# Optimization experiments

Hardware: AMD Instinct MI355X
Metric: run time of the kernel (lower is better)

## Reference

```python
import jax, jax.numpy as jnp
import numpy as np

V = 1024      # visible_size (channel_size)
H = 2048      # hidden_size
F = V + H     # full_size
T = 64        # timesteps
REC = 0.8     # params['lambda']


def setup_inputs() -> dict:
    key = jax.random.key(0)
    k1, k2, k3 = jax.random.split(key, 3)
    X = jax.random.normal(k1, (T, V), jnp.float32)
    # scale W so tanh does not fully saturate (fan-in scaling, like default init)
    W = jax.random.normal(k2, (F, F), jnp.float32) / np.float32(np.sqrt(F))
    b = jax.random.normal(k3, (F,), jnp.float32) * 0.01
    # Lambda: visible block = REC, hidden block = 1, diagonal of visible block = 1
    lam = jnp.concatenate(
        [jnp.full((V, V), REC, jnp.float32), jnp.ones((V, H), jnp.float32)], axis=1
    )
    lam = lam.at[jnp.arange(V), jnp.arange(V)].set(1.0)
    return {"X": X, "W": W, "b": b, "lam": lam}


def reference(X, W, b, lam):
    v = lam.shape[0]           # visible size
    one_minus_lam_vis = 1.0 - lam[:, :v]  # zero outside visible block anyway

    def step(carry, x_t):
        R, _ = carry
        WR = R @ W.T + b                      # [V, F] Linear applied row-wise
        U = lam * WR                          # gated recurrent part
        # I has x_t broadcast across rows in the visible block, zeros elsewhere
        U = U.at[:, :v].add(one_minus_lam_vis * x_t[None, :])
        R_next = jnp.tanh(U)                  # phi = torch.tanh
        return (R_next, U), None

    R0 = jnp.zeros((v, W.shape[0]), X.dtype)
    (_, U_last), _ = jax.lax.scan(step, (R0, R0), X)
    # torch.diag(U[:, :visible]) -> diagonal entries, shape [V]
    idx = jnp.arange(v)
    return U_last[idx, idx]
```

## Files before the change

kernel.cpp:

```cpp
#include <hip/hip_runtime.h>
#include <math.h>

#define V 1024
#define H 2048
#define F 3072
#define T 64
#define REC 0.8f

#define BM 128
#define BN 128
#define KT16 (F / 16)
#define NSS  (KT16 / 4)

typedef _Float16 half8 __attribute__((ext_vector_type(8)));
typedef float floatx16 __attribute__((ext_vector_type(16)));

__device__ __forceinline__ void gld16(const void* g, void* l) {
    __builtin_amdgcn_global_load_lds(
        (const __attribute__((address_space(1))) void*)g,
        (__attribute__((address_space(3))) void*)l, 16, 0, 0);
}

__device__ __forceinline__ float fast_tanh(float u) {
    float e = __expf(2.f * u);
    return 1.f - 2.f * __builtin_amdgcn_rcpf(e + 1.f);
}


__global__ __launch_bounds__(256)
void conv_w_fm(const float* __restrict__ W, _Float16* __restrict__ Wfm) {
    const int ct = blockIdx.y;
    const int ix = blockIdx.x * 256 + threadIdx.x;
    const int kt = ix >> 8;
    const int q  = ix & 255;
    const int n  = ct * 128 + ((q >> 6) & 3) * 32 + (q & 31);
    const int k0 = kt * 16 + ((q >> 5) & 1) * 8;
    const float* src = W + (size_t)n * F + k0;
    float4 v0 = *(const float4*)src;
    float4 v1 = *(const float4*)(src + 4);
    half8 o = { (_Float16)v0.x, (_Float16)v0.y, (_Float16)v0.z, (_Float16)v0.w,
                (_Float16)v1.x, (_Float16)v1.y, (_Float16)v1.z, (_Float16)v1.w };
    *(half8*)(Wfm + ((size_t)(ct * KT16 + kt) * 2048 + q * 8)) = o;
}

__global__ __launch_bounds__(256)
void init_step0(const float* __restrict__ b, const float* __restrict__ x0,
                _Float16* __restrict__ Rfm) {
    const int rt = blockIdx.y;
    const int ix = blockIdx.x * 256 + threadIdx.x;
    const int kt = ix >> 8;
    const int q  = ix & 255;
    const int gi = rt * 128 + ((q >> 6) & 3) * 32 + (q & 31);
    const int k0 = kt * 16 + ((q >> 5) & 1) * 8;
    half8 o;
    #pragma unroll
    for (int e = 0; e < 8; ++e) {
        int gj = k0 + e;
        float wr = b[gj];
        float u = (gj >= V || gi == gj) ? wr : (REC * wr + (1.f - REC) * x0[gj]);
        o[e] = (_Float16)fast_tanh(u);
    }
    *(half8*)(Rfm + ((size_t)(rt * KT16 + kt) * 2048 + q * 8)) = o;
}

__global__ __launch_bounds__(512, 2)
void frnn_step(const _Float16* __restrict__ Rin, const _Float16* __restrict__ Wfm,
               const float* __restrict__ b, const float* __restrict__ xt,
               _Float16* __restrict__ Rout, float* __restrict__ out, int is_last)
{
    __shared__ _Float16 A0[8192], B0[8192];
    __shared__ _Float16 A1[8192], B1[8192];
    __shared__ _Float16 A2[8192], B2[8192];

    const int tid  = threadIdx.x;
    const int lane = tid & 63;
    const int wid  = tid >> 6;
    const int sp   = wid & 1;
    const int kg   = wid >> 1;
    const int row0 = blockIdx.y * BM;
    const int col0 = blockIdx.x * BN;
    const int lane8 = lane * 8;

    const int sq  = tid & 255;
    const int sq8 = sq * 8;
    const _Float16* sgbase = (tid < 256)
        ? Rin + ((size_t)blockIdx.y * KT16 * 2048 + sq8)
        : Wfm + ((size_t)blockIdx.x * KT16 * 2048 + sq8);

    floatx16 acc[2][4];
    #pragma unroll
    for (int i = 0; i < 2; ++i)
        #pragma unroll
        for (int j = 0; j < 4; ++j)
            #pragma unroll
            for (int r = 0; r < 16; ++r) acc[i][j][r] = 0.f;

    {
        _Float16* d0 = (tid < 256) ? &A0[sq8] : &B0[sq8];
        _Float16* d1 = (tid < 256) ? &A1[sq8] : &B1[sq8];
        #pragma unroll
        for (int g = 0; g < 4; ++g)
            gld16(sgbase + (size_t)g * 2048, d0 + g * 2048);
        asm volatile("" ::: "memory");
        #pragma unroll
        for (int g = 0; g < 4; ++g)
            gld16(sgbase + (size_t)(4 + g) * 2048, d1 + g * 2048);
    }

#define BODY(M, CA, CB, NA, NB)                                                 \
  {                                                                             \
    asm volatile("s_waitcnt vmcnt(4) lgkmcnt(0)\n\ts_barrier" ::: "memory");    \
    const _Float16* sA = &CA[kg * 2048];                                        \
    const _Float16* sB = &CB[kg * 2048];                                        \
    half8 a0 = *(const half8*)(sA + sp * 1024 + lane8);                         \
    half8 a1 = *(const half8*)(sA + sp * 1024 + 512 + lane8);                   \
    half8 b0 = *(const half8*)(sB + lane8);                                     \
    half8 b1 = *(const half8*)(sB + 512 + lane8);                               \
    half8 b2 = *(const half8*)(sB + 1024 + lane8);                              \
    half8 b3 = *(const half8*)(sB + 1536 + lane8);                              \
    asm volatile("" ::: "memory");           \
    int nxt = (M) + 2; if (nxt >= NSS) nxt -= NSS;     \
    _Float16* dst = (tid < 256) ? &NA[sq8] : &NB[sq8];                          \
    _Pragma("unroll")                                                           \
    for (int g = 0; g < 4; ++g)                                                 \
        gld16(sgbase + (size_t)(nxt * 4 + g) * 2048, dst + g * 2048);           \
    acc[0][0] = __builtin_amdgcn_mfma_f32_32x32x16_f16(a0, b0, acc[0][0],0,0,0);\
    acc[0][1] = __builtin_amdgcn_mfma_f32_32x32x16_f16(a0, b1, acc[0][1],0,0,0);\
    acc[0][2] = __builtin_amdgcn_mfma_f32_32x32x16_f16(a0, b2, acc[0][2],0,0,0);\
    acc[0][3] = __builtin_amdgcn_mfma_f32_32x32x16_f16(a0, b3, acc[0][3],0,0,0);\
    acc[1][0] = __builtin_amdgcn_mfma_f32_32x32x16_f16(a1, b0, acc[1][0],0,0,0);\
    acc[1][1] = __builtin_amdgcn_mfma_f32_32x32x16_f16(a1, b1, acc[1][1],0,0,0);\
    acc[1][2] = __builtin_amdgcn_mfma_f32_32x32x16_f16(a1, b2, acc[1][2],0,0,0);\
    acc[1][3] = __builtin_amdgcn_mfma_f32_32x32x16_f16(a1, b3, acc[1][3],0,0,0);\
  }

    #pragma unroll 1
    for (int m3 = 0; m3 < NSS / 3; ++m3) {
        const int M = m3 * 3;
        BODY(M,     A0, B0, A2, B2)
        BODY(M + 1, A1, B1, A0, B0)
        BODY(M + 2, A2, B2, A1, B1)
    }
#undef BODY

    asm volatile("s_waitcnt vmcnt(0) lgkmcnt(0)\n\ts_barrier" ::: "memory");

    const int m32 = lane & 31, hh = lane >> 5;
    float b_r[4], x_r[4];
    if (kg == 0) {
        #pragma unroll
        for (int j = 0; j < 4; ++j) {
            int gj = col0 + j * 32 + m32;
            b_r[j] = b[gj];
            x_r[j] = (gj < V) ? xt[gj] : 0.f;
        }
    }

    float* red0 = (float*)(sp ? A1 : A0);
    float* red1 = (float*)(sp ? B1 : B0);
    #pragma unroll 1
    for (int w = 1; w < 4; ++w) {
        if (kg == w) {
            #pragma unroll
            for (int j = 0; j < 4; ++j)
                #pragma unroll
                for (int q4 = 0; q4 < 4; ++q4) {
                    float4 v0 = { acc[0][j][4*q4],   acc[0][j][4*q4+1],
                                  acc[0][j][4*q4+2], acc[0][j][4*q4+3] };
                    float4 v1 = { acc[1][j][4*q4],   acc[1][j][4*q4+1],
                                  acc[1][j][4*q4+2], acc[1][j][4*q4+3] };
                    *(float4*)(red0 + (j*4 + q4) * 256 + lane * 4) = v0;
                    *(float4*)(red1 + (j*4 + q4) * 256 + lane * 4) = v1;
                }
        }
        __syncthreads();
        if (kg == 0) {
            #pragma unroll
            for (int j = 0; j < 4; ++j)
                #pragma unroll
                for (int q4 = 0; q4 < 4; ++q4) {
                    float4 v0 = *(const float4*)(red0 + (j*4 + q4) * 256 + lane * 4);
                    float4 v1 = *(const float4*)(red1 + (j*4 + q4) * 256 + lane * 4);
                    acc[0][j][4*q4]   += v0.x; acc[0][j][4*q4+1] += v0.y;
                    acc[0][j][4*q4+2] += v0.z; acc[0][j][4*q4+3] += v0.w;
                    acc[1][j][4*q4]   += v1.x; acc[1][j][4*q4+1] += v1.y;
                    acc[1][j][4*q4+2] += v1.z; acc[1][j][4*q4+3] += v1.w;
                }
        }
        __syncthreads();
    }

    if (kg == 0) {
        #pragma unroll
        for (int i = 0; i < 2; ++i) {
            const int mb = sp * 2 + i;
            #pragma unroll
            for (int j = 0; j < 4; ++j) {
                const int gj = col0 + j * 32 + m32;
                const int kt = gj >> 4;
                const int h2 = (gj >> 3) & 1;
                const int e  = gj & 7;
                _Float16* tb = Rout + ((size_t)(blockIdx.y * KT16 + kt) * 2048
                                       + (mb * 2 + h2) * 256 + e);
                const float bj = b_r[j];
                const float xj = x_r[j];
                const bool vis = (gj < V);
                #pragma unroll
                for (int r = 0; r < 16; ++r) {
                    const int mrow = 4 * hh + (r & 3) + 8 * (r >> 2);
                    const int gi = row0 + mb * 32 + mrow;
                    float wr = acc[i][j][r] + bj;
                    float u = (!vis || gi == gj) ? wr : (REC * wr + (1.f - REC) * xj);
                    tb[mrow * 8] = (_Float16)fast_tanh(u);
                    if (is_last && gi == gj) out[gi] = u;
                }
            }
        }
    }
}

extern "C" void kernel_launch(void* const* d_in, const int* in_sizes, int n_in,
                              void* d_out, int out_size, void* d_ws, size_t ws_size,
                              hipStream_t stream) {
    const float* X = (const float*)d_in[0];
    const float* W = (const float*)d_in[1];
    const float* b = (const float*)d_in[2];
    float* out = (float*)d_out;

    _Float16* Wfm = (_Float16*)d_ws;
    _Float16* Ra  = Wfm + (size_t)F * F;
    _Float16* Rb  = Ra + (size_t)V * F;

    conv_w_fm<<<dim3(192, 24), 256, 0, stream>>>(W, Wfm);
    init_step0<<<dim3(192, 8), 256, 0, stream>>>(b, X, Ra);

    for (int t = 1; t < T; ++t) {
        _Float16* Rin  = (t & 1) ? Ra : Rb;
        _Float16* Rout = (t & 1) ? Rb : Ra;
        frnn_step<<<dim3(24, 8), 512, 0, stream>>>(Rin, Wfm, b, X + (size_t)t * V,
                                                   Rout, out, t == T - 1);
    }
}
```

Before: 2.082 ms.

## Double-buffer LDS fragments in registers and deepen global prefetch to three stages

Adds a register-level double buffer: each iteration loads the next stage's A/B fragments from LDS while issuing MFMAs on fragments loaded in the previous iteration. The global-to-LDS prefetch distance grows from two to three stages, the main loop is unrolled by six to rotate both buffers, and MFMA issue is wrapped in s_setprio and a sched_barrier. The aim is to hide LDS read latency behind the matrix cores, at the cost of more VGPRs and possible occupancy loss. With three LDS buffers and a prefetch distance of three, the buffer being refilled may still be read by lagging waves, since the barrier only covers the previous stage.

```diff
diff --git a/kernel.cpp b/kernel.cpp
--- a/kernel.cpp
+++ b/kernel.cpp
@@ -95,6 +95,8 @@
             #pragma unroll
             for (int r = 0; r < 16; ++r) acc[i][j][r] = 0.f;
 
+    half8 fa0[2], fa1[2], fb0[2], fb1[2], fb2[2], fb3[2];
+
     {
         _Float16* d0 = (tid < 256) ? &A0[sq8] : &B0[sq8];
         _Float16* d1 = (tid < 256) ? &A1[sq8] : &B1[sq8];
@@ -105,41 +107,65 @@
         #pragma unroll
         for (int g = 0; g < 4; ++g)
             gld16(sgbase + (size_t)(4 + g) * 2048, d1 + g * 2048);
-    }
-
-#define BODY(M, CA, CB, NA, NB)                                                 \
+        asm volatile("" ::: "memory");
+    }
+    {
+        asm volatile("s_waitcnt vmcnt(4) lgkmcnt(0)\n\ts_barrier" ::: "memory");
+        const _Float16* sA = &A0[kg * 2048];
+        const _Float16* sB = &B0[kg * 2048];
+        fa0[0] = *(const half8*)(sA + sp * 1024 + lane8);
+        fa1[0] = *(const half8*)(sA + sp * 1024 + 512 + lane8);
+        fb0[0] = *(const half8*)(sB + lane8);
+        fb1[0] = *(const half8*)(sB + 512 + lane8);
+        fb2[0] = *(const half8*)(sB + 1024 + lane8);
+        fb3[0] = *(const half8*)(sB + 1536 + lane8);
+        asm volatile("" ::: "memory");
+        _Float16* d2 = (tid < 256) ? &A2[sq8] : &B2[sq8];
+        #pragma unroll
+        for (int g = 0; g < 4; ++g)
+            gld16(sgbase + (size_t)(8 + g) * 2048, d2 + g * 2048);
+        asm volatile("" ::: "memory");
+    }
+
+#define BODY(M, RA, RB, NA, NB, RS, CS)                                         \
   {                                                                             \
     asm volatile("s_waitcnt vmcnt(4) lgkmcnt(0)\n\ts_barrier" ::: "memory");    \
-    const _Float16* sA = &CA[kg * 2048];                                        \
-    const _Float16* sB = &CB[kg * 2048];                                        \
-    half8 a0 = *(const half8*)(sA + sp * 1024 + lane8);                         \
-    half8 a1 = *(const half8*)(sA + sp * 1024 + 512 + lane8);                   \
-    half8 b0 = *(const half8*)(sB + lane8);                                     \
-    half8 b1 = *(const half8*)(sB + 512 + lane8);                               \
-    half8 b2 = *(const half8*)(sB + 1024 + lane8);                              \
-    half8 b3 = *(const half8*)(sB + 1536 + lane8);                              \
-    asm volatile("" ::: "memory");           \
-    int nxt = (M) + 2; if (nxt >= NSS) nxt -= NSS;     \
+    const _Float16* sA = &RA[kg * 2048];                                        \
+    const _Float16* sB = &RB[kg * 2048];                                        \
+    fa0[RS] = *(const half8*)(sA + sp * 1024 + lane8);                          \
+    fa1[RS] = *(const half8*)(sA + sp * 1024 + 512 + lane8);                    \
+    fb0[RS] = *(const half8*)(sB + lane8);                                      \
+    fb1[RS] = *(const half8*)(sB + 512 + lane8);                                \
+    fb2[RS] = *(const half8*)(sB + 1024 + lane8);                               \
+    fb3[RS] = *(const half8*)(sB + 1536 + lane8);                               \
+    asm volatile("" ::: "memory");          \
+    int nxt = (M) + 3; if (nxt >= NSS) nxt -= NSS;     \
     _Float16* dst = (tid < 256) ? &NA[sq8] : &NB[sq8];                          \
     _Pragma("unroll")                                                           \
     for (int g = 0; g < 4; ++g)                                                 \
         gld16(sgbase + (size_t)(nxt * 4 + g) * 2048, dst + g * 2048);           \
-    acc[0][0] = __builtin_amdgcn_mfma_f32_32x32x16_f16(a0, b0, acc[0][0],0,0,0);\
-    acc[0][1] = __builtin_amdgcn_mfma_f32_32x32x16_f16(a0, b1, acc[0][1],0,0,0);\
-    acc[0][2] = __builtin_amdgcn_mfma_f32_32x32x16_f16(a0, b2, acc[0][2],0,0,0);\
-    acc[0][3] = __builtin_amdgcn_mfma_f32_32x32x16_f16(a0, b3, acc[0][3],0,0,0);\
-    acc[1][0] = __builtin_amdgcn_mfma_f32_32x32x16_f16(a1, b0, acc[1][0],0,0,0);\
-    acc[1][1] = __builtin_amdgcn_mfma_f32_32x32x16_f16(a1, b1, acc[1][1],0,0,0);\
-    acc[1][2] = __builtin_amdgcn_mfma_f32_32x32x16_f16(a1, b2, acc[1][2],0,0,0);\
-    acc[1][3] = __builtin_amdgcn_mfma_f32_32x32x16_f16(a1, b3, acc[1][3],0,0,0);\
+    __builtin_amdgcn_sched_barrier(0);      \
+    __builtin_amdgcn_s_setprio(1);                                              \
+    acc[0][0] = __builtin_amdgcn_mfma_f32_32x32x16_f16(fa0[CS], fb0[CS], acc[0][0],0,0,0);\
+    acc[0][1] = __builtin_amdgcn_mfma_f32_32x32x16_f16(fa0[CS], fb1[CS], acc[0][1],0,0,0);\
+    acc[0][2] = __builtin_amdgcn_mfma_f32_32x32x16_f16(fa0[CS], fb2[CS], acc[0][2],0,0,0);\
+    acc[0][3] = __builtin_amdgcn_mfma_f32_32x32x16_f16(fa0[CS], fb3[CS], acc[0][3],0,0,0);\
+    acc[1][0] = __builtin_amdgcn_mfma_f32_32x32x16_f16(fa1[CS], fb0[CS], acc[1][0],0,0,0);\
+    acc[1][1] = __builtin_amdgcn_mfma_f32_32x32x16_f16(fa1[CS], fb1[CS], acc[1][1],0,0,0);\
+    acc[1][2] = __builtin_amdgcn_mfma_f32_32x32x16_f16(fa1[CS], fb2[CS], acc[1][2],0,0,0);\
+    acc[1][3] = __builtin_amdgcn_mfma_f32_32x32x16_f16(fa1[CS], fb3[CS], acc[1][3],0,0,0);\
+    __builtin_amdgcn_s_setprio(0);                                              \
   }
 
     #pragma unroll 1
-    for (int m3 = 0; m3 < NSS / 3; ++m3) {
-        const int M = m3 * 3;
-        BODY(M,     A0, B0, A2, B2)
-        BODY(M + 1, A1, B1, A0, B0)
-        BODY(M + 2, A2, B2, A1, B1)
+    for (int m6 = 0; m6 < NSS / 6; ++m6) {
+        const int M = m6 * 6;
+        BODY(M,     A1, B1, A0, B0, 1, 0)
+        BODY(M + 1, A2, B2, A1, B1, 0, 1)
+        BODY(M + 2, A0, B0, A2, B2, 1, 0)
+        BODY(M + 3, A1, B1, A0, B0, 0, 1)
+        BODY(M + 4, A2, B2, A1, B1, 1, 0)
+        BODY(M + 5, A0, B0, A2, B2, 0, 1)
     }
 #undef BODY
 
```

New measurement: 2.103 ms. About the same (+1.0%).

## Load MFMA fragments directly from global into registers, drop LDS staging

Applied to the files above, without the earlier changes.

Each warp now reads its A and B fragments straight from global memory into a three-deep register ring, replacing the shared LDS triple buffer that was filled with global_load_lds and guarded by a barrier on every k-step. Each warp also takes a contiguous quarter of the K range (kg*KTW) instead of interleaving. MFMA issue is wrapped in s_setprio to favour the math waves. This removes the per-step barriers and LDS traffic, but data shared between the two sp warps is no longer reused through LDS, so global and L2 load traffic goes up and each lane needs more registers, which may lower occupancy.

```diff
diff --git a/kernel.cpp b/kernel.cpp
--- a/kernel.cpp
+++ b/kernel.cpp
@@ -10,16 +10,10 @@
 #define BM 128
 #define BN 128
 #define KT16 (F / 16)
-#define NSS  (KT16 / 4)
+#define KTW  (KT16 / 4)
 
 typedef _Float16 half8 __attribute__((ext_vector_type(8)));
 typedef float floatx16 __attribute__((ext_vector_type(16)));
-
-__device__ __forceinline__ void gld16(const void* g, void* l) {
-    __builtin_amdgcn_global_load_lds(
-        (const __attribute__((address_space(1))) void*)g,
-        (__attribute__((address_space(3))) void*)l, 16, 0, 0);
-}
 
 __device__ __forceinline__ float fast_tanh(float u) {
     float e = __expf(2.f * u);
@@ -68,9 +62,7 @@
                const float* __restrict__ b, const float* __restrict__ xt,
                _Float16* __restrict__ Rout, float* __restrict__ out, int is_last)
 {
-    __shared__ _Float16 A0[8192], B0[8192];
-    __shared__ _Float16 A1[8192], B1[8192];
-    __shared__ _Float16 A2[8192], B2[8192];
+    __shared__ float red[16384];
 
     const int tid  = threadIdx.x;
     const int lane = tid & 63;
@@ -80,12 +72,11 @@
     const int row0 = blockIdx.y * BM;
     const int col0 = blockIdx.x * BN;
     const int lane8 = lane * 8;
-
-    const int sq  = tid & 255;
-    const int sq8 = sq * 8;
-    const _Float16* sgbase = (tid < 256)
-        ? Rin + ((size_t)blockIdx.y * KT16 * 2048 + sq8)
-        : Wfm + ((size_t)blockIdx.x * KT16 * 2048 + sq8);
+    const int kg48 = kg * KTW;
+
+    const _Float16* abase = Rin + ((size_t)blockIdx.y * KT16 * 2048
+                                   + sp * 1024 + lane8);
+    const _Float16* bbase = Wfm + ((size_t)blockIdx.x * KT16 * 2048 + lane8);
 
     floatx16 acc[2][4];
     #pragma unroll
@@ -95,55 +86,49 @@
             #pragma unroll
             for (int r = 0; r < 16; ++r) acc[i][j][r] = 0.f;
 
-    {
-        _Float16* d0 = (tid < 256) ? &A0[sq8] : &B0[sq8];
-        _Float16* d1 = (tid < 256) ? &A1[sq8] : &B1[sq8];
-        #pragma unroll
-        for (int g = 0; g < 4; ++g)
-            gld16(sgbase + (size_t)g * 2048, d0 + g * 2048);
-        asm volatile("" ::: "memory");
-        #pragma unroll
-        for (int g = 0; g < 4; ++g)
-            gld16(sgbase + (size_t)(4 + g) * 2048, d1 + g * 2048);
-    }
-
-#define BODY(M, CA, CB, NA, NB)                                                 \
+    half8 fa0[3], fa1[3], fb0[3], fb1[3], fb2[3], fb3[3];
+
+#define LOADK(S, KTI)                                                           \
   {                                                                             \
-    asm volatile("s_waitcnt vmcnt(4) lgkmcnt(0)\n\ts_barrier" ::: "memory");    \
-    const _Float16* sA = &CA[kg * 2048];                                        \
-    const _Float16* sB = &CB[kg * 2048];                                        \
-    half8 a0 = *(const half8*)(sA + sp * 1024 + lane8);                         \
-    half8 a1 = *(const half8*)(sA + sp * 1024 + 512 + lane8);                   \
-    half8 b0 = *(const half8*)(sB + lane8);                                     \
-    half8 b1 = *(const half8*)(sB + 512 + lane8);                               \
-    half8 b2 = *(const half8*)(sB + 1024 + lane8);                              \
-    half8 b3 = *(const half8*)(sB + 1536 + lane8);                              \
-    asm volatile("" ::: "memory");           \
-    int nxt = (M) + 2; if (nxt >= NSS) nxt -= NSS;     \
-    _Float16* dst = (tid < 256) ? &NA[sq8] : &NB[sq8];                          \
-    _Pragma("unroll")                                                           \
-    for (int g = 0; g < 4; ++g)                                                 \
-        gld16(sgbase + (size_t)(nxt * 4 + g) * 2048, dst + g * 2048);           \
-    acc[0][0] = __builtin_amdgcn_mfma_f32_32x32x16_f16(a0, b0, acc[0][0],0,0,0);\
-    acc[0][1] = __builtin_amdgcn_mfma_f32_32x32x16_f16(a0, b1, acc[0][1],0,0,0);\
-    acc[0][2] = __builtin_amdgcn_mfma_f32_32x32x16_f16(a0, b2, acc[0][2],0,0,0);\
-    acc[0][3] = __builtin_amdgcn_mfma_f32_32x32x16_f16(a0, b3, acc[0][3],0,0,0);\
-    acc[1][0] = __builtin_amdgcn_mfma_f32_32x32x16_f16(a1, b0, acc[1][0],0,0,0);\
-    acc[1][1] = __builtin_amdgcn_mfma_f32_32x32x16_f16(a1, b1, acc[1][1],0,0,0);\
-    acc[1][2] = __builtin_amdgcn_mfma_f32_32x32x16_f16(a1, b2, acc[1][2],0,0,0);\
-    acc[1][3] = __builtin_amdgcn_mfma_f32_32x32x16_f16(a1, b3, acc[1][3],0,0,0);\
+    const size_t off = (size_t)(kg48 + (KTI)) * 2048;                           \
+    const _Float16* ap = abase + off;                                           \
+    const _Float16* bp = bbase + off;                                           \
+    fa0[S] = *(const half8*)ap;                                                 \
+    fa1[S] = *(const half8*)(ap + 512);                                         \
+    fb0[S] = *(const half8*)bp;                                                 \
+    fb1[S] = *(const half8*)(bp + 512);                                         \
+    fb2[S] = *(const half8*)(bp + 1024);                                        \
+    fb3[S] = *(const half8*)(bp + 1536);                                        \
   }
 
+    LOADK(0, 0)
+    LOADK(1, 1)
+
+#define BODY(S, PFS, JJ)                                                        \
+  {                                                                             \
+    int pj = (JJ) + 2; if (pj > KTW - 1) pj = KTW - 1;                          \
+    LOADK(PFS, pj)                                                              \
+    __builtin_amdgcn_s_setprio(1);                                              \
+    acc[0][0] = __builtin_amdgcn_mfma_f32_32x32x16_f16(fa0[S], fb0[S], acc[0][0],0,0,0);\
+    acc[0][1] = __builtin_amdgcn_mfma_f32_32x32x16_f16(fa0[S], fb1[S], acc[0][1],0,0,0);\
+    acc[0][2] = __builtin_amdgcn_mfma_f32_32x32x16_f16(fa0[S], fb2[S], acc[0][2],0,0,0);\
+    acc[0][3] = __builtin_amdgcn_mfma_f32_32x32x16_f16(fa0[S], fb3[S], acc[0][3],0,0,0);\
+    acc[1][0] = __builtin_amdgcn_mfma_f32_32x32x16_f16(fa1[S], fb0[S], acc[1][0],0,0,0);\
+    acc[1][1] = __builtin_amdgcn_mfma_f32_32x32x16_f16(fa1[S], fb1[S], acc[1][1],0,0,0);\
+    acc[1][2] = __builtin_amdgcn_mfma_f32_32x32x16_f16(fa1[S], fb2[S], acc[1][2],0,0,0);\
+    acc[1][3] = __builtin_amdgcn_mfma_f32_32x32x16_f16(fa1[S], fb3[S], acc[1][3],0,0,0);\
+    __builtin_amdgcn_s_setprio(0);                                              \
+  }
+
     #pragma unroll 1
-    for (int m3 = 0; m3 < NSS / 3; ++m3) {
-        const int M = m3 * 3;
-        BODY(M,     A0, B0, A2, B2)
-        BODY(M + 1, A1, B1, A0, B0)
-        BODY(M + 2, A2, B2, A1, B1)
+    for (int j3 = 0; j3 < KTW / 3; ++j3) {
+        const int JJ = j3 * 3;
+        BODY(0, 2, JJ)
+        BODY(1, 0, JJ + 1)
+        BODY(2, 1, JJ + 2)
     }
 #undef BODY
-
-    asm volatile("s_waitcnt vmcnt(0) lgkmcnt(0)\n\ts_barrier" ::: "memory");
+#undef LOADK
 
     const int m32 = lane & 31, hh = lane >> 5;
     float b_r[4], x_r[4];
@@ -156,8 +141,8 @@
         }
     }
 
-    float* red0 = (float*)(sp ? A1 : A0);
-    float* red1 = (float*)(sp ? B1 : B0);
+    float* red0 = &red[sp * 8192];
+    float* red1 = &red[sp * 8192 + 4096];
     #pragma unroll 1
     for (int w = 1; w < 4; ++w) {
         if (kg == w) {
```

New measurement: 2.333 ms. 12.0% more time.

## Retile recurrent GEMM to 64x96 blocks with 256 threads for better CU fill

Applied to the files above, without the earlier changes.

Changes the per-step GEMM tile from 128x128 (512 threads) to 64x96 (256 threads), giving 512 blocks instead of 192 to better occupy all compute units. The fragment-major layouts for W and R, the staging loads, the wait counts and the split-K reduction are rewritten to match the new tile shape. The trade-off is more redundant global/L2 traffic, since each operand tile is re-read by more blocks.

```diff
diff --git a/kernel.cpp b/kernel.cpp
--- a/kernel.cpp
+++ b/kernel.cpp
@@ -7,10 +7,11 @@
 #define T 64
 #define REC 0.8f
 
-#define BM 128
-#define BN 128
+#define BM 64
+#define BN 96
 #define KT16 (F / 16)
 #define NSS  (KT16 / 4)
+
 
 typedef _Float16 half8 __attribute__((ext_vector_type(8)));
 typedef float floatx16 __attribute__((ext_vector_type(16)));
@@ -26,21 +27,20 @@
     return 1.f - 2.f * __builtin_amdgcn_rcpf(e + 1.f);
 }
 
-
 __global__ __launch_bounds__(256)
 void conv_w_fm(const float* __restrict__ W, _Float16* __restrict__ Wfm) {
     const int ct = blockIdx.y;
     const int ix = blockIdx.x * 256 + threadIdx.x;
-    const int kt = ix >> 8;
-    const int q  = ix & 255;
-    const int n  = ct * 128 + ((q >> 6) & 3) * 32 + (q & 31);
+    const int kt = ix / 192;
+    const int q  = ix % 192;
+    const int n  = ct * 96 + ((q >> 6) & 3) * 32 + (q & 31);
     const int k0 = kt * 16 + ((q >> 5) & 1) * 8;
     const float* src = W + (size_t)n * F + k0;
     float4 v0 = *(const float4*)src;
     float4 v1 = *(const float4*)(src + 4);
     half8 o = { (_Float16)v0.x, (_Float16)v0.y, (_Float16)v0.z, (_Float16)v0.w,
                 (_Float16)v1.x, (_Float16)v1.y, (_Float16)v1.z, (_Float16)v1.w };
-    *(half8*)(Wfm + ((size_t)(ct * KT16 + kt) * 2048 + q * 8)) = o;
+    *(half8*)(Wfm + ((size_t)(ct * KT16 + kt) * 1536 + q * 8)) = o;
 }
 
 __global__ __launch_bounds__(256)
@@ -48,9 +48,9 @@
                 _Float16* __restrict__ Rfm) {
     const int rt = blockIdx.y;
     const int ix = blockIdx.x * 256 + threadIdx.x;
-    const int kt = ix >> 8;
-    const int q  = ix & 255;
-    const int gi = rt * 128 + ((q >> 6) & 3) * 32 + (q & 31);
+    const int kt = ix >> 7;
+    const int q  = ix & 127;
+    const int gi = rt * 64 + ((q >> 6) & 1) * 32 + (q & 31);
     const int k0 = kt * 16 + ((q >> 5) & 1) * 8;
     half8 o;
     #pragma unroll
@@ -60,132 +60,131 @@
         float u = (gj >= V || gi == gj) ? wr : (REC * wr + (1.f - REC) * x0[gj]);
         o[e] = (_Float16)fast_tanh(u);
     }
-    *(half8*)(Rfm + ((size_t)(rt * KT16 + kt) * 2048 + q * 8)) = o;
-}
-
-__global__ __launch_bounds__(512, 2)
+    *(half8*)(Rfm + ((size_t)(rt * KT16 + kt) * 1024 + q * 8)) = o;
+}
+
+__global__ __launch_bounds__(256, 2)
 void frnn_step(const _Float16* __restrict__ Rin, const _Float16* __restrict__ Wfm,
                const float* __restrict__ b, const float* __restrict__ xt,
                _Float16* __restrict__ Rout, float* __restrict__ out, int is_last)
 {
-    __shared__ _Float16 A0[8192], B0[8192];
-    __shared__ _Float16 A1[8192], B1[8192];
-    __shared__ _Float16 A2[8192], B2[8192];
+    __shared__ _Float16 lds[30720];
 
     const int tid  = threadIdx.x;
     const int lane = tid & 63;
-    const int wid  = tid >> 6;
-    const int sp   = wid & 1;
-    const int kg   = wid >> 1;
+    const int kg   = tid >> 6;
     const int row0 = blockIdx.y * BM;
     const int col0 = blockIdx.x * BN;
     const int lane8 = lane * 8;
 
-    const int sq  = tid & 255;
+    const int sq  = tid & 127;
     const int sq8 = sq * 8;
-    const _Float16* sgbase = (tid < 256)
-        ? Rin + ((size_t)blockIdx.y * KT16 * 2048 + sq8)
-        : Wfm + ((size_t)blockIdx.x * KT16 * 2048 + sq8);
-
-    floatx16 acc[2][4];
+    const bool isA = (tid < 128);
+    const _Float16* sgbase = isA
+        ? Rin + ((size_t)blockIdx.y * KT16 * 1024 + sq8)
+        : Wfm + ((size_t)blockIdx.x * KT16 * 1536 + sq8);
+
+    floatx16 acc[2][3];
     #pragma unroll
     for (int i = 0; i < 2; ++i)
         #pragma unroll
-        for (int j = 0; j < 4; ++j)
+        for (int j = 0; j < 3; ++j)
             #pragma unroll
             for (int r = 0; r < 16; ++r) acc[i][j][r] = 0.f;
 
-    {
-        _Float16* d0 = (tid < 256) ? &A0[sq8] : &B0[sq8];
-        _Float16* d1 = (tid < 256) ? &A1[sq8] : &B1[sq8];
-        #pragma unroll
-        for (int g = 0; g < 4; ++g)
-            gld16(sgbase + (size_t)g * 2048, d0 + g * 2048);
-        asm volatile("" ::: "memory");
-        #pragma unroll
-        for (int g = 0; g < 4; ++g)
-            gld16(sgbase + (size_t)(4 + g) * 2048, d1 + g * 2048);
-    }
-
-#define BODY(M, CA, CB, NA, NB)                                                 \
+#define STAGE(P, SS)                                                            \
+  do {                                                                          \
+    if (isA) {                                                                  \
+        _Float16* d = &lds[(P) * 10240 + sq8];                                  \
+        const _Float16* s = sgbase + (size_t)(SS) * 4096;                       \
+        _Pragma("unroll")                                                       \
+        for (int g = 0; g < 4; ++g) gld16(s + g * 1024, d + g * 1024);          \
+    } else {                                                                    \
+        _Float16* d = &lds[(P) * 10240 + 4096 + sq8];                           \
+        const _Float16* s = sgbase + (size_t)(SS) * 6144;                       \
+        _Pragma("unroll")                                                       \
+        for (int g = 0; g < 6; ++g) gld16(s + g * 1024, d + g * 1024);          \
+    }                                                                           \
+  } while (0)
+
+    STAGE(0, 0);
+    asm volatile("" ::: "memory");
+    STAGE(1, 1);
+    asm volatile("" ::: "memory");
+
+#define BODY(M, PR, PW)                                                         \
   {                                                                             \
-    asm volatile("s_waitcnt vmcnt(4) lgkmcnt(0)\n\ts_barrier" ::: "memory");    \
-    const _Float16* sA = &CA[kg * 2048];                                        \
-    const _Float16* sB = &CB[kg * 2048];                                        \
-    half8 a0 = *(const half8*)(sA + sp * 1024 + lane8);                         \
-    half8 a1 = *(const half8*)(sA + sp * 1024 + 512 + lane8);                   \
+    if (kg < 2) asm volatile("s_waitcnt vmcnt(4) lgkmcnt(0)" ::: "memory");     \
+    else        asm volatile("s_waitcnt vmcnt(6) lgkmcnt(0)" ::: "memory");     \
+    asm volatile("s_barrier" ::: "memory");                                     \
+    const _Float16* sA = &lds[(PR) * 10240 + kg * 1024];                        \
+    const _Float16* sB = &lds[(PR) * 10240 + 4096 + kg * 1536];                 \
+    half8 a0 = *(const half8*)(sA + lane8);                                     \
+    half8 a1 = *(const half8*)(sA + 512 + lane8);                               \
     half8 b0 = *(const half8*)(sB + lane8);                                     \
     half8 b1 = *(const half8*)(sB + 512 + lane8);                               \
     half8 b2 = *(const half8*)(sB + 1024 + lane8);                              \
-    half8 b3 = *(const half8*)(sB + 1536 + lane8);                              \
     asm volatile("" ::: "memory");           \
     int nxt = (M) + 2; if (nxt >= NSS) nxt -= NSS;     \
-    _Float16* dst = (tid < 256) ? &NA[sq8] : &NB[sq8];                          \
-    _Pragma("unroll")                                                           \
-    for (int g = 0; g < 4; ++g)                                                 \
-        gld16(sgbase + (size_t)(nxt * 4 + g) * 2048, dst + g * 2048);           \
+    STAGE(PW, nxt);                                                             \
     acc[0][0] = __builtin_amdgcn_mfma_f32_32x32x16_f16(a0, b0, acc[0][0],0,0,0);\
     acc[0][1] = __builtin_amdgcn_mfma_f32_32x32x16_f16(a0, b1, acc[0][1],0,0,0);\
     acc[0][2] = __builtin_amdgcn_mfma_f32_32x32x16_f16(a0, b2, acc[0][2],0,0,0);\
-    acc[0][3] = __builtin_amdgcn_mfma_f32_32x32x16_f16(a0, b3, acc[0][3],0,0,0);\
     acc[1][0] = __builtin_amdgcn_mfma_f32_32x32x16_f16(a1, b0, acc[1][0],0,0,0);\
     acc[1][1] = __builtin_amdgcn_mfma_f32_32x32x16_f16(a1, b1, acc[1][1],0,0,0);\
     acc[1][2] = __builtin_amdgcn_mfma_f32_32x32x16_f16(a1, b2, acc[1][2],0,0,0);\
-    acc[1][3] = __builtin_amdgcn_mfma_f32_32x32x16_f16(a1, b3, acc[1][3],0,0,0);\
   }
 
     #pragma unroll 1
     for (int m3 = 0; m3 < NSS / 3; ++m3) {
         const int M = m3 * 3;
-        BODY(M,     A0, B0, A2, B2)
-        BODY(M + 1, A1, B1, A0, B0)
-        BODY(M + 2, A2, B2, A1, B1)
+        BODY(M,     0, 2)
+        BODY(M + 1, 1, 0)
+        BODY(M + 2, 2, 1)
     }
 #undef BODY
+#undef STAGE
 
     asm volatile("s_waitcnt vmcnt(0) lgkmcnt(0)\n\ts_barrier" ::: "memory");
 
     const int m32 = lane & 31, hh = lane >> 5;
-    float b_r[4], x_r[4];
+    float b_r[3], x_r[3];
     if (kg == 0) {
         #pragma unroll
-        for (int j = 0; j < 4; ++j) {
+        for (int j = 0; j < 3; ++j) {
             int gj = col0 + j * 32 + m32;
             b_r[j] = b[gj];
             x_r[j] = (gj < V) ? xt[gj] : 0.f;
         }
     }
 
-    float* red0 = (float*)(sp ? A1 : A0);
-    float* red1 = (float*)(sp ? B1 : B0);
+    float* red = (float*)lds;
     #pragma unroll 1
     for (int w = 1; w < 4; ++w) {
         if (kg == w) {
             #pragma unroll
-            for (int j = 0; j < 4; ++j)
+            for (int i = 0; i < 2; ++i)
                 #pragma unroll
-                for (int q4 = 0; q4 < 4; ++q4) {
-                    float4 v0 = { acc[0][j][4*q4],   acc[0][j][4*q4+1],
-                                  acc[0][j][4*q4+2], acc[0][j][4*q4+3] };
-                    float4 v1 = { acc[1][j][4*q4],   acc[1][j][4*q4+1],
-                                  acc[1][j][4*q4+2], acc[1][j][4*q4+3] };
-                    *(float4*)(red0 + (j*4 + q4) * 256 + lane * 4) = v0;
-                    *(float4*)(red1 + (j*4 + q4) * 256 + lane * 4) = v1;
-                }
+                for (int j = 0; j < 3; ++j)
+                    #pragma unroll
+                    for (int q4 = 0; q4 < 4; ++q4) {
+                        float4 v = { acc[i][j][4*q4],   acc[i][j][4*q4+1],
+                                     acc[i][j][4*q4+2], acc[i][j][4*q4+3] };
+                        *(float4*)(red + ((i*3 + j)*4 + q4) * 256 + lane * 4) = v;
+                    }
         }
         __syncthreads();
         if (kg == 0) {
             #pragma unroll
-            for (int j = 0; j < 4; ++j)
+            for (int i = 0; i < 2; ++i)
                 #pragma unroll
-                for (int q4 = 0; q4 < 4; ++q4) {
-                    float4 v0 = *(const float4*)(red0 + (j*4 + q4) * 256 + lane * 4);
-                    float4 v1 = *(const float4*)(red1 + (j*4 + q4) * 256 + lane * 4);
-                    acc[0][j][4*q4]   += v0.x; acc[0][j][4*q4+1] += v0.y;
-                    acc[0][j][4*q4+2] += v0.z; acc[0][j][4*q4+3] += v0.w;
-                    acc[1][j][4*q4]   += v1.x; acc[1][j][4*q4+1] += v1.y;
-                    acc[1][j][4*q4+2] += v1.z; acc[1][j][4*q4+3] += v1.w;
-                }
+                for (int j = 0; j < 3; ++j)
+                    #pragma unroll
+                    for (int q4 = 0; q4 < 4; ++q4) {
+                        float4 v = *(const float4*)(red + ((i*3 + j)*4 + q4) * 256 + lane * 4);
+                        acc[i][j][4*q4]   += v.x; acc[i][j][4*q4+1] += v.y;
+                        acc[i][j][4*q4+2] += v.z; acc[i][j][4*q4+3] += v.w;
+                    }
         }
         __syncthreads();
     }
@@ -193,22 +192,21 @@
     if (kg == 0) {
         #pragma unroll
         for (int i = 0; i < 2; ++i) {
-            const int mb = sp * 2 + i;
-            #pragma unroll
-            for (int j = 0; j < 4; ++j) {
+            #pragma unroll
+            for (int j = 0; j < 3; ++j) {
                 const int gj = col0 + j * 32 + m32;
                 const int kt = gj >> 4;
                 const int h2 = (gj >> 3) & 1;
                 const int e  = gj & 7;
-                _Float16* tb = Rout + ((size_t)(blockIdx.y * KT16 + kt) * 2048
-                                       + (mb * 2 + h2) * 256 + e);
+                _Float16* tb = Rout + ((size_t)(blockIdx.y * KT16 + kt) * 1024
+                                       + (i * 64 + h2 * 32) * 8 + e);
                 const float bj = b_r[j];
                 const float xj = x_r[j];
                 const bool vis = (gj < V);
                 #pragma unroll
                 for (int r = 0; r < 16; ++r) {
                     const int mrow = 4 * hh + (r & 3) + 8 * (r >> 2);
-                    const int gi = row0 + mb * 32 + mrow;
+                    const int gi = row0 + i * 32 + mrow;
                     float wr = acc[i][j][r] + bj;
                     float u = (!vis || gi == gj) ? wr : (REC * wr + (1.f - REC) * xj);
                     tb[mrow * 8] = (_Float16)fast_tanh(u);
@@ -231,13 +229,13 @@
     _Float16* Ra  = Wfm + (size_t)F * F;
     _Float16* Rb  = Ra + (size_t)V * F;
 
-    conv_w_fm<<<dim3(192, 24), 256, 0, stream>>>(W, Wfm);
-    init_step0<<<dim3(192, 8), 256, 0, stream>>>(b, X, Ra);
+    conv_w_fm<<<dim3(144, 32), 256, 0, stream>>>(W, Wfm);
+    init_step0<<<dim3(96, 16), 256, 0, stream>>>(b, X, Ra);
 
     for (int t = 1; t < T; ++t) {
         _Float16* Rin  = (t & 1) ? Ra : Rb;
         _Float16* Rout = (t & 1) ? Rb : Ra;
-        frnn_step<<<dim3(24, 8), 512, 0, stream>>>(Rin, Wfm, b, X + (size_t)t * V,
-                                                   Rout, out, t == T - 1);
-    }
-}
+        frnn_step<<<dim3(32, 16), 256, 0, stream>>>(Rin, Wfm, b, X + (size_t)t * V,
+                                                    Rout, out, t == T - 1);
+    }
+}
```

Measured after the change: 2.138 ms. +2.6%, slower.
